# Optimization experiments

Measured on AMD Instinct MI355X. Metric: run time of the kernel, lower is better.

Reference implementation:

```python
import jax, jax.numpy as jnp
import numpy as np

B, T, I, H = 64, 1024, 256, 512


def setup_inputs() -> dict:
    key = jax.random.key(0)
    ks = jax.random.split(key, 5)
    s = 1.0 / np.sqrt(H)  # PyTorch LSTM init scale (uniform(-s, s)); we use scaled normal
    return {
        "x": jax.random.normal(ks[0], (B, T, I), dtype=jnp.float32),
        "w_ih": jax.random.normal(ks[1], (4 * H, I), dtype=jnp.float32) * s,
        "w_hh": jax.random.normal(ks[2], (4 * H, H), dtype=jnp.float32) * s,
        "b_ih": jax.random.normal(ks[3], (4 * H,), dtype=jnp.float32) * s,
        "b_hh": jax.random.normal(ks[4], (4 * H,), dtype=jnp.float32) * s,
    }


def _lstm(x, w_ih, w_hh, b_ih, b_hh):
    # x: [B, T, I]. Precompute input projections for all timesteps at once.
    pre = jnp.einsum("bti,gi->btg", x, w_ih) + b_ih + b_hh  # [B, T, 4H]
    pre = jnp.swapaxes(pre, 0, 1)  # [T, B, 4H] for scan over time

    h0 = jnp.zeros((x.shape[0], H), dtype=x.dtype)
    c0 = jnp.zeros((x.shape[0], H), dtype=x.dtype)

    def step(carry, pre_t):
        h, c = carry
        gates = pre_t + h @ w_hh.T  # [B, 4H]
        i, f, g, o = jnp.split(gates, 4, axis=-1)  # PyTorch gate order: i, f, g, o
        i = jax.nn.sigmoid(i)
        f = jax.nn.sigmoid(f)
        g = jnp.tanh(g)
        o = jax.nn.sigmoid(o)
        c = f * c + i * g
        h = o * jnp.tanh(c)
        return (h, c), h

    (h_n, c_n), hs = jax.lax.scan(step, (h0, c0), pre)
    out = jnp.swapaxes(hs, 0, 1)  # [B, T, H] (batch_first=True)
    return out, (h_n[None], c_n[None])  # h_n/c_n: [num_layers=1, B, H]


def reference(x, w_ih, w_hh, b_ih, b_hh):
    return _lstm(x, w_ih, w_hh, b_ih, b_hh)
```

## Files before the change

kernel.cpp:

```cpp
#include <hip/hip_runtime.h>
#include <cstdint>
#include <cstddef>


#define NBATCH 64
#define TSTEPS 1024
#define IDIM   256
#define HDIM   512
#define KDIM   768
#define WS     776
#define ABUF_USHORT (16 * WS)
#define SMEM_BYTES  (2 * ABUF_USHORT * 2)

#define HB_WORDS 32768

typedef __attribute__((ext_vector_type(8))) short short8x;
typedef __attribute__((ext_vector_type(4))) float f32x4;

__device__ __forceinline__ float sigmoid_f(float v) {
    return 1.0f / (1.0f + __expf(-v));
}
__device__ __forceinline__ float tanh_f(float v) {
    float a = fabsf(v);
    float e = __expf(-2.0f * a);
    float r = (1.0f - e) / (1.0f + e);
    return v >= 0.0f ? r : -r;
}
__device__ __forceinline__ unsigned short f2bf(float f) {
    unsigned int u = __float_as_uint(f);
    return (unsigned short)((u + 0x7fffu + ((u >> 16) & 1u)) >> 16);
}
__device__ __forceinline__ unsigned long long pack4(float4 v) {
    unsigned long long b0 = f2bf(v.x), b1 = f2bf(v.y), b2 = f2bf(v.z), b3 = f2bf(v.w);
    return b0 | (b1 << 16) | (b2 << 32) | (b3 << 48);
}

__global__ void __launch_bounds__(256, 1) lstm_persistent(
    const float* __restrict__ x,
    const float* __restrict__ w_ih,
    const float* __restrict__ w_hh,
    const float* __restrict__ b_ih,
    const float* __restrict__ b_hh,
    float* __restrict__ out,
    unsigned int* __restrict__ h_tb)
{
    const int tid = threadIdx.x;
    const int wg  = blockIdx.x;
    const int bg  = wg >> 4;
    const int hg  = wg & 15;

    extern __shared__ char smem[];
    unsigned short* a0 = (unsigned short*)smem;
    unsigned short* a1 = a0 + ABUF_USHORT;

    const int wv   = tid >> 6;
    const int lane = tid & 63;
    const int ln   = lane & 15;
    const int q    = lane >> 4;

    short8x af0[24], af1[24];
    float bias0[4], bias1[4];
    #pragma unroll
    for (int tau = 0; tau < 2; ++tau) {
        const int T  = wv * 2 + tau;
        const int gr = (ln & 3) * HDIM + hg * 32 + T * 4 + (ln >> 2);
        #pragma unroll
        for (int s = 0; s < 24; ++s) {
            const float* src = (s < 8)
                ? (w_ih + (size_t)gr * IDIM + (s * 32 + q * 8))
                : (w_hh + (size_t)gr * HDIM + ((s - 8) * 32 + q * 8));
            float4 v0 = *(const float4*)(src);
            float4 v1 = *(const float4*)(src + 4);
            union { short8x v; unsigned long long u[2]; } tmp;
            tmp.u[0] = pack4(v0);
            tmp.u[1] = pack4(v1);
            if (tau == 0) af0[s] = tmp.v; else af1[s] = tmp.v;
        }
        const int hid = hg * 32 + T * 4 + q;
        #pragma unroll
        for (int j = 0; j < 4; ++j) {
            float bv = b_ih[j * HDIM + hid] + b_hh[j * HDIM + hid];
            if (tau == 0) bias0[j] = bv; else bias1[j] = bv;
        }
    }

    const int sn  = tid >> 4;
    const int sj  = tid & 15;
    const int gbn = bg * 16 + sn;
    const float* xbase = x + (size_t)gbn * TSTEPS * IDIM + sj * 16;

    const size_t hb_lane = (size_t)(bg * 16 + ln) * HDIM + hg * 32 + wv * 8 + q;
    float c0 = 0.0f, c1 = 0.0f, h0f = 0.0f, h1f = 0.0f;

    const unsigned long long tagmask = 0xffff0000ffff0000ull;

    for (int t = 0; t < TSTEPS; ++t) {
        unsigned short* abuf = (t & 1) ? a1 : a0;
        unsigned short* axp  = abuf + sn * WS + sj * 16;
        unsigned short* ahp  = abuf + sn * WS + IDIM + sj * 32;

        {
            const float* xp = xbase + (size_t)t * IDIM;
            float4 v0 = *(const float4*)(xp);
            float4 v1 = *(const float4*)(xp + 4);
            float4 v2 = *(const float4*)(xp + 8);
            float4 v3 = *(const float4*)(xp + 12);
            *(unsigned long long*)(axp + 0)  = pack4(v0);
            *(unsigned long long*)(axp + 4)  = pack4(v1);
            *(unsigned long long*)(axp + 8)  = pack4(v2);
            *(unsigned long long*)(axp + 12) = pack4(v3);
        }

        if (t > 0) {
            const unsigned long long* hp = (const unsigned long long*)
                (h_tb + (size_t)(t & 1) * HB_WORDS + (size_t)gbn * HDIM + sj * 32);
            unsigned long long hv[16];
            const unsigned long long tagpat =
                ((unsigned long long)(unsigned)t << 48) |
                ((unsigned long long)(unsigned)t << 16);
            unsigned pend = 0xffffu;
            while (pend) {
                unsigned np = 0;
                #pragma unroll
                for (int u = 0; u < 16; ++u) {
                    if (pend & (1u << u)) {
                        hv[u] = __hip_atomic_load(hp + u, __ATOMIC_RELAXED,
                                                  __HIP_MEMORY_SCOPE_AGENT);
                    }
                }
                #pragma unroll
                for (int u = 0; u < 16; ++u) {
                    if ((pend & (1u << u)) && (hv[u] & tagmask) != tagpat)
                        np |= (1u << u);
                }
                pend = np;
            }
            unsigned int pk[16];
            #pragma unroll
            for (int u = 0; u < 16; ++u) {
                pk[u] = (unsigned int)(hv[u] & 0xffffu)
                      | ((unsigned int)((hv[u] >> 32) & 0xffffu) << 16);
            }
            unsigned int* ahp32 = (unsigned int*)ahp;
            #pragma unroll
            for (int v = 0; v < 4; ++v) {
                uint4 w4 = make_uint4(pk[4*v], pk[4*v+1], pk[4*v+2], pk[4*v+3]);
                *(uint4*)(ahp32 + 4*v) = w4;
            }
            if (sn == ((hg + t) & 15)) {
                float* op = out + ((size_t)gbn * TSTEPS + (t - 1)) * HDIM + sj * 32;
                #pragma unroll
                for (int v = 0; v < 8; ++v) {
                    unsigned int w0 = pk[2*v], w1 = pk[2*v+1];
                    f32x4 f4;
                    f4[0] = __uint_as_float(w0 << 16);
                    f4[1] = __uint_as_float(w0 & 0xffff0000u);
                    f4[2] = __uint_as_float(w1 << 16);
                    f4[3] = __uint_as_float(w1 & 0xffff0000u);
                    __builtin_nontemporal_store(f4, (f32x4*)(op + 4*v));
                }
            }
        } else {
            unsigned int* ahp32 = (unsigned int*)ahp;
            uint4 z = make_uint4(0u, 0u, 0u, 0u);
            #pragma unroll
            for (int v = 0; v < 4; ++v) *(uint4*)(ahp32 + 4*v) = z;
        }
        __syncthreads();

        const unsigned short* Bbase = abuf + (size_t)ln * WS + q * 8;
        f32x4 acc0 = {0.f, 0.f, 0.f, 0.f};
        f32x4 acc1 = {0.f, 0.f, 0.f, 0.f};
        #pragma unroll
        for (int s = 0; s < 24; ++s) {
            short8x bf = *(const short8x*)(Bbase + s * 32);
            acc0 = __builtin_amdgcn_mfma_f32_16x16x32_bf16(af0[s], bf, acc0, 0, 0, 0);
            acc1 = __builtin_amdgcn_mfma_f32_16x16x32_bf16(af1[s], bf, acc1, 0, 0, 0);
        }

        const unsigned int tagw = (unsigned int)(t + 1) << 16;
        unsigned int* hb = h_tb + (size_t)((t + 1) & 1) * HB_WORDS + hb_lane;
        {
            float ig = sigmoid_f(acc0[0] + bias0[0]);
            float fg = sigmoid_f(acc0[1] + bias0[1]);
            float gt = tanh_f   (acc0[2] + bias0[2]);
            float og = sigmoid_f(acc0[3] + bias0[3]);
            c0  = fg * c0 + ig * gt;
            h0f = og * tanh_f(c0);
            __hip_atomic_store(hb, tagw | (unsigned int)f2bf(h0f),
                               __ATOMIC_RELAXED, __HIP_MEMORY_SCOPE_AGENT);
        }
        {
            float ig = sigmoid_f(acc1[0] + bias1[0]);
            float fg = sigmoid_f(acc1[1] + bias1[1]);
            float gt = tanh_f   (acc1[2] + bias1[2]);
            float og = sigmoid_f(acc1[3] + bias1[3]);
            c1  = fg * c1 + ig * gt;
            h1f = og * tanh_f(c1);
            __hip_atomic_store(hb + 4, tagw | (unsigned int)f2bf(h1f),
                               __ATOMIC_RELAXED, __HIP_MEMORY_SCOPE_AGENT);
        }
    }

    {
        const size_t HN_OFF = (size_t)NBATCH * TSTEPS * HDIM;
        const size_t CN_OFF = HN_OFF + (size_t)NBATCH * HDIM;
        const int gb   = bg * 16 + ln;
        const int hid0 = hg * 32 + wv * 8 + q;
        out[((size_t)gb * TSTEPS + (TSTEPS - 1)) * HDIM + hid0]     = h0f;
        out[((size_t)gb * TSTEPS + (TSTEPS - 1)) * HDIM + hid0 + 4] = h1f;
        out[HN_OFF + (size_t)gb * HDIM + hid0]     = h0f;
        out[HN_OFF + (size_t)gb * HDIM + hid0 + 4] = h1f;
        out[CN_OFF + (size_t)gb * HDIM + hid0]     = c0;
        out[CN_OFF + (size_t)gb * HDIM + hid0 + 4] = c1;
    }
}

extern "C" void kernel_launch(void* const* d_in, const int* in_sizes, int n_in,
                              void* d_out, int out_size, void* d_ws, size_t ws_size,
                              hipStream_t stream) {
    const float* x    = (const float*)d_in[0];
    const float* w_ih = (const float*)d_in[1];
    const float* w_hh = (const float*)d_in[2];
    const float* b_ih = (const float*)d_in[3];
    const float* b_hh = (const float*)d_in[4];
    float* out = (float*)d_out;

    unsigned int* h_tb = (unsigned int*)d_ws;

    (void)hipFuncSetAttribute((const void*)lstm_persistent,
                        hipFuncAttributeMaxDynamicSharedMemorySize, SMEM_BYTES);

    void* args[] = {(void*)&x, (void*)&w_ih, (void*)&w_hh, (void*)&b_ih,
                    (void*)&b_hh, (void*)&out, (void*)&h_tb};
    hipError_t err = hipLaunchCooperativeKernel((void*)lstm_persistent,
                                                dim3(64), dim3(256), args,
                                                SMEM_BYTES, stream);
    if (err != hipSuccess) {
        hipLaunchKernelGGL(lstm_persistent, dim3(64), dim3(256), SMEM_BYTES,
                           stream, x, w_ih, w_hh, b_ih, b_hh, out, h_tb);
    }
}
```

Baseline: 5.477 ms.

## Halve workgroups to 32, four hidden tiles per wave, vectorized tagged h exchange

Repartitions the persistent LSTM from 64 to 32 workgroups, so each wave holds four weight fragment sets in registers and computes 64 hidden units per workgroup. The h-exchange is rewritten with dwordx4 sc0/sc1 loads and stores of tagged words, and the bias moves to shared memory. The aim is fewer participants in the per-step cross-workgroup sync and fewer, wider memory transactions. The cost is doubled per-step MFMA work per workgroup, higher register pressure (96 fragment vectors), and fewer CUs in use.

```diff
diff --git a/kernel.cpp b/kernel.cpp
--- a/kernel.cpp
+++ b/kernel.cpp
@@ -10,12 +10,14 @@
 #define KDIM   768
 #define WS     776
 #define ABUF_USHORT (16 * WS)
-#define SMEM_BYTES  (2 * ABUF_USHORT * 2)
+#define BIAS_OFF    (2 * ABUF_USHORT * 2)
+#define SMEM_BYTES  (BIAS_OFF + 1024)
 
 #define HB_WORDS 32768
 
 typedef __attribute__((ext_vector_type(8))) short short8x;
 typedef __attribute__((ext_vector_type(4))) float f32x4;
+typedef __attribute__((ext_vector_type(4))) unsigned int u32x4;
 
 __device__ __forceinline__ float sigmoid_f(float v) {
     return 1.0f / (1.0f + __expf(-v));
@@ -33,6 +35,9 @@
 __device__ __forceinline__ unsigned long long pack4(float4 v) {
     unsigned long long b0 = f2bf(v.x), b1 = f2bf(v.y), b2 = f2bf(v.z), b3 = f2bf(v.w);
     return b0 | (b1 << 16) | (b2 << 32) | (b3 << 48);
+}
+__device__ __forceinline__ unsigned int pklo(unsigned int a, unsigned int b) {
+    return (a & 0xffffu) | (b << 16);
 }
 
 __global__ void __launch_bounds__(256, 1) lstm_persistent(
@@ -46,42 +51,49 @@
 {
     const int tid = threadIdx.x;
     const int wg  = blockIdx.x;
-    const int bg  = wg >> 4;
-    const int hg  = wg & 15;
+    const int bg  = wg >> 3;
+    const int hg  = wg & 7;
 
     extern __shared__ char smem[];
     unsigned short* a0 = (unsigned short*)smem;
     unsigned short* a1 = a0 + ABUF_USHORT;
+    float* bias_s = (float*)(smem + BIAS_OFF);
 
     const int wv   = tid >> 6;
     const int lane = tid & 63;
     const int ln   = lane & 15;
     const int q    = lane >> 4;
 
-    short8x af0[24], af1[24];
-    float bias0[4], bias1[4];
-    #pragma unroll
-    for (int tau = 0; tau < 2; ++tau) {
-        const int T  = wv * 2 + tau;
-        const int gr = (ln & 3) * HDIM + hg * 32 + T * 4 + (ln >> 2);
+    short8x af0[24], af1[24], af2[24], af3[24];
+    {
+        const int grb = (ln & 3) * HDIM + hg * 64 + wv * 16 + (ln >> 2) * 4;
+#define LOADW(AF, TAU)                                                        \
+        {                                                                     \
+            const int gr = grb + (TAU);                                       \
+            _Pragma("unroll")                                                 \
+            for (int s = 0; s < 24; ++s) {                                    \
+                const float* src = (s < 8)                                    \
+                    ? (w_ih + (size_t)gr * IDIM + (s * 32 + q * 8))           \
+                    : (w_hh + (size_t)gr * HDIM + ((s - 8) * 32 + q * 8));    \
+                float4 v0 = *(const float4*)(src);                            \
+                float4 v1 = *(const float4*)(src + 4);                        \
+                union { short8x v; unsigned long long u[2]; } tmp;            \
+                tmp.u[0] = pack4(v0);                                         \
+                tmp.u[1] = pack4(v1);                                         \
+                AF[s] = tmp.v;                                                \
+            }                                                                 \
+        }
+        LOADW(af0, 0) LOADW(af1, 1) LOADW(af2, 2) LOADW(af3, 3)
+#undef LOADW
+    }
+
+    if (ln < 4) {
+        const int tau = ln;
+        const int hid = hg * 64 + wv * 16 + q * 4 + tau;
         #pragma unroll
-        for (int s = 0; s < 24; ++s) {
-            const float* src = (s < 8)
-                ? (w_ih + (size_t)gr * IDIM + (s * 32 + q * 8))
-                : (w_hh + (size_t)gr * HDIM + ((s - 8) * 32 + q * 8));
-            float4 v0 = *(const float4*)(src);
-            float4 v1 = *(const float4*)(src + 4);
-            union { short8x v; unsigned long long u[2]; } tmp;
-            tmp.u[0] = pack4(v0);
-            tmp.u[1] = pack4(v1);
-            if (tau == 0) af0[s] = tmp.v; else af1[s] = tmp.v;
-        }
-        const int hid = hg * 32 + T * 4 + q;
-        #pragma unroll
-        for (int j = 0; j < 4; ++j) {
-            float bv = b_ih[j * HDIM + hid] + b_hh[j * HDIM + hid];
-            if (tau == 0) bias0[j] = bv; else bias1[j] = bv;
-        }
+        for (int j = 0; j < 4; ++j)
+            bias_s[(wv * 4 + q) * 16 + tau * 4 + j] =
+                b_ih[j * HDIM + hid] + b_hh[j * HDIM + hid];
     }
 
     const int sn  = tid >> 4;
@@ -89,15 +101,14 @@
     const int gbn = bg * 16 + sn;
     const float* xbase = x + (size_t)gbn * TSTEPS * IDIM + sj * 16;
 
-    const size_t hb_lane = (size_t)(bg * 16 + ln) * HDIM + hg * 32 + wv * 8 + q;
-    float c0 = 0.0f, c1 = 0.0f, h0f = 0.0f, h1f = 0.0f;
-
-    const unsigned long long tagmask = 0xffff0000ffff0000ull;
+    const size_t hb_off = (size_t)(bg * 16 + ln) * HDIM + hg * 64 + wv * 16 + q * 4;
+    float c0 = 0.f, c1 = 0.f, c2 = 0.f, c3 = 0.f;
+    float hf0 = 0.f, hf1 = 0.f, hf2 = 0.f, hf3 = 0.f;
 
     for (int t = 0; t < TSTEPS; ++t) {
         unsigned short* abuf = (t & 1) ? a1 : a0;
         unsigned short* axp  = abuf + sn * WS + sj * 16;
-        unsigned short* ahp  = abuf + sn * WS + IDIM + sj * 32;
+        unsigned int*   ahp32 = (unsigned int*)(abuf + sn * WS + IDIM + sj * 32);
 
         {
             const float* xp = xbase + (size_t)t * IDIM;
@@ -112,93 +123,100 @@
         }
 
         if (t > 0) {
-            const unsigned long long* hp = (const unsigned long long*)
-                (h_tb + (size_t)(t & 1) * HB_WORDS + (size_t)gbn * HDIM + sj * 32);
-            unsigned long long hv[16];
-            const unsigned long long tagpat =
-                ((unsigned long long)(unsigned)t << 48) |
-                ((unsigned long long)(unsigned)t << 16);
-            unsigned pend = 0xffffu;
+            const unsigned int* hp =
+                h_tb + (size_t)(t & 1) * HB_WORDS + (size_t)gbn * HDIM + sj * 32;
+            u32x4 hv[8];
+            const unsigned int tagw = (unsigned int)t << 16;
+            unsigned pend = 0xffu;
             while (pend) {
+                #pragma unroll
+                for (int u = 0; u < 8; ++u) {
+                    if (pend & (1u << u)) {
+                        asm volatile("global_load_dwordx4 %0, %1, off sc0 sc1"
+                                     : "=v"(hv[u]) : "v"(hp + u * 4) : "memory");
+                    }
+                }
+                asm volatile("s_waitcnt vmcnt(0)" ::: "memory");
+                __builtin_amdgcn_sched_barrier(0);
                 unsigned np = 0;
                 #pragma unroll
-                for (int u = 0; u < 16; ++u) {
+                for (int u = 0; u < 8; ++u) {
                     if (pend & (1u << u)) {
-                        hv[u] = __hip_atomic_load(hp + u, __ATOMIC_RELAXED,
-                                                  __HIP_MEMORY_SCOPE_AGENT);
+                        unsigned m = ((hv[u][0] ^ tagw) | (hv[u][1] ^ tagw) |
+                                      (hv[u][2] ^ tagw) | (hv[u][3] ^ tagw))
+                                     & 0xffff0000u;
+                        if (m) np |= (1u << u);
                     }
-                }
-                #pragma unroll
-                for (int u = 0; u < 16; ++u) {
-                    if ((pend & (1u << u)) && (hv[u] & tagmask) != tagpat)
-                        np |= (1u << u);
                 }
                 pend = np;
             }
-            unsigned int pk[16];
-            #pragma unroll
-            for (int u = 0; u < 16; ++u) {
-                pk[u] = (unsigned int)(hv[u] & 0xffffu)
-                      | ((unsigned int)((hv[u] >> 32) & 0xffffu) << 16);
-            }
-            unsigned int* ahp32 = (unsigned int*)ahp;
             #pragma unroll
             for (int v = 0; v < 4; ++v) {
-                uint4 w4 = make_uint4(pk[4*v], pk[4*v+1], pk[4*v+2], pk[4*v+3]);
-                *(uint4*)(ahp32 + 4*v) = w4;
+                u32x4 a = hv[2 * v], b = hv[2 * v + 1];
+                u32x4 w4;
+                w4[0] = pklo(a[0], a[1]);
+                w4[1] = pklo(a[2], a[3]);
+                w4[2] = pklo(b[0], b[1]);
+                w4[3] = pklo(b[2], b[3]);
+                *(u32x4*)(ahp32 + 4 * v) = w4;
             }
-            if (sn == ((hg + t) & 15)) {
+            if ((sn & 7) == ((hg + t) & 7)) {
                 float* op = out + ((size_t)gbn * TSTEPS + (t - 1)) * HDIM + sj * 32;
                 #pragma unroll
-                for (int v = 0; v < 8; ++v) {
-                    unsigned int w0 = pk[2*v], w1 = pk[2*v+1];
+                for (int u = 0; u < 8; ++u) {
+                    u32x4 h4 = hv[u];
                     f32x4 f4;
-                    f4[0] = __uint_as_float(w0 << 16);
-                    f4[1] = __uint_as_float(w0 & 0xffff0000u);
-                    f4[2] = __uint_as_float(w1 << 16);
-                    f4[3] = __uint_as_float(w1 & 0xffff0000u);
-                    __builtin_nontemporal_store(f4, (f32x4*)(op + 4*v));
+                    f4[0] = __uint_as_float(h4[0] << 16);
+                    f4[1] = __uint_as_float(h4[1] << 16);
+                    f4[2] = __uint_as_float(h4[2] << 16);
+                    f4[3] = __uint_as_float(h4[3] << 16);
+                    __builtin_nontemporal_store(f4, (f32x4*)(op + 4 * u));
                 }
             }
         } else {
-            unsigned int* ahp32 = (unsigned int*)ahp;
-            uint4 z = make_uint4(0u, 0u, 0u, 0u);
+            u32x4 z = {0u, 0u, 0u, 0u};
             #pragma unroll
-            for (int v = 0; v < 4; ++v) *(uint4*)(ahp32 + 4*v) = z;
+            for (int v = 0; v < 4; ++v) *(u32x4*)(ahp32 + 4 * v) = z;
         }
         __syncthreads();
 
         const unsigned short* Bbase = abuf + (size_t)ln * WS + q * 8;
-        f32x4 acc0 = {0.f, 0.f, 0.f, 0.f};
-        f32x4 acc1 = {0.f, 0.f, 0.f, 0.f};
+        f32x4 ac0 = {0.f, 0.f, 0.f, 0.f};
+        f32x4 ac1 = {0.f, 0.f, 0.f, 0.f};
+        f32x4 ac2 = {0.f, 0.f, 0.f, 0.f};
+        f32x4 ac3 = {0.f, 0.f, 0.f, 0.f};
         #pragma unroll
         for (int s = 0; s < 24; ++s) {
             short8x bf = *(const short8x*)(Bbase + s * 32);
-            acc0 = __builtin_amdgcn_mfma_f32_16x16x32_bf16(af0[s], bf, acc0, 0, 0, 0);
-            acc1 = __builtin_amdgcn_mfma_f32_16x16x32_bf16(af1[s], bf, acc1, 0, 0, 0);
-        }
-
-        const unsigned int tagw = (unsigned int)(t + 1) << 16;
-        unsigned int* hb = h_tb + (size_t)((t + 1) & 1) * HB_WORDS + hb_lane;
+            ac0 = __builtin_amdgcn_mfma_f32_16x16x32_bf16(af0[s], bf, ac0, 0, 0, 0);
+            ac1 = __builtin_amdgcn_mfma_f32_16x16x32_bf16(af1[s], bf, ac1, 0, 0, 0);
+            ac2 = __builtin_amdgcn_mfma_f32_16x16x32_bf16(af2[s], bf, ac2, 0, 0, 0);
+            ac3 = __builtin_amdgcn_mfma_f32_16x16x32_bf16(af3[s], bf, ac3, 0, 0, 0);
+        }
+
+        const unsigned int tagw1 = (unsigned int)(t + 1) << 16;
+        const float* bsl = bias_s + (wv * 4 + q) * 16;
+        u32x4 pub;
+#define ACT(ACC, TAU, CREF, HREF)                                             \
+        {                                                                     \
+            f32x4 bs = *(const f32x4*)(bsl + (TAU) * 4);                      \
+            float ig = sigmoid_f(ACC[0] + bs[0]);                             \
+            float fg = sigmoid_f(ACC[1] + bs[1]);                             \
+            float gt = tanh_f   (ACC[2] + bs[2]);                             \
+            float og = sigmoid_f(ACC[3] + bs[3]);                             \
+            CREF = fg * CREF + ig * gt;                                       \
+            HREF = og * tanh_f(CREF);                                         \
+            pub[TAU] = tagw1 | (unsigned int)f2bf(HREF);                      \
+        }
+        ACT(ac0, 0, c0, hf0)
+        ACT(ac1, 1, c1, hf1)
+        ACT(ac2, 2, c2, hf2)
+        ACT(ac3, 3, c3, hf3)
+#undef ACT
         {
-            float ig = sigmoid_f(acc0[0] + bias0[0]);
-            float fg = sigmoid_f(acc0[1] + bias0[1]);
-            float gt = tanh_f   (acc0[2] + bias0[2]);
-            float og = sigmoid_f(acc0[3] + bias0[3]);
-            c0  = fg * c0 + ig * gt;
-            h0f = og * tanh_f(c0);
-            __hip_atomic_store(hb, tagw | (unsigned int)f2bf(h0f),
-                               __ATOMIC_RELAXED, __HIP_MEMORY_SCOPE_AGENT);
-        }
-        {
-            float ig = sigmoid_f(acc1[0] + bias1[0]);
-            float fg = sigmoid_f(acc1[1] + bias1[1]);
-            float gt = tanh_f   (acc1[2] + bias1[2]);
-            float og = sigmoid_f(acc1[3] + bias1[3]);
-            c1  = fg * c1 + ig * gt;
-            h1f = og * tanh_f(c1);
-            __hip_atomic_store(hb + 4, tagw | (unsigned int)f2bf(h1f),
-                               __ATOMIC_RELAXED, __HIP_MEMORY_SCOPE_AGENT);
+            unsigned int* hb = h_tb + (size_t)((t + 1) & 1) * HB_WORDS + hb_off;
+            asm volatile("global_store_dwordx4 %0, %1, off sc0 sc1"
+                         :: "v"(hb), "v"(pub) : "memory");
         }
     }
 
@@ -206,13 +224,12 @@
         const size_t HN_OFF = (size_t)NBATCH * TSTEPS * HDIM;
         const size_t CN_OFF = HN_OFF + (size_t)NBATCH * HDIM;
         const int gb   = bg * 16 + ln;
-        const int hid0 = hg * 32 + wv * 8 + q;
-        out[((size_t)gb * TSTEPS + (TSTEPS - 1)) * HDIM + hid0]     = h0f;
-        out[((size_t)gb * TSTEPS + (TSTEPS - 1)) * HDIM + hid0 + 4] = h1f;
-        out[HN_OFF + (size_t)gb * HDIM + hid0]     = h0f;
-        out[HN_OFF + (size_t)gb * HDIM + hid0 + 4] = h1f;
-        out[CN_OFF + (size_t)gb * HDIM + hid0]     = c0;
-        out[CN_OFF + (size_t)gb * HDIM + hid0 + 4] = c1;
+        const int hid0 = hg * 64 + wv * 16 + q * 4;
+        f32x4 hv4 = {hf0, hf1, hf2, hf3};
+        f32x4 cv4 = {c0, c1, c2, c3};
+        *(f32x4*)(out + ((size_t)gb * TSTEPS + (TSTEPS - 1)) * HDIM + hid0) = hv4;
+        *(f32x4*)(out + HN_OFF + (size_t)gb * HDIM + hid0) = hv4;
+        *(f32x4*)(out + CN_OFF + (size_t)gb * HDIM + hid0) = cv4;
     }
 }
 
@@ -234,10 +251,10 @@
     void* args[] = {(void*)&x, (void*)&w_ih, (void*)&w_hh, (void*)&b_ih,
                     (void*)&b_hh, (void*)&out, (void*)&h_tb};
     hipError_t err = hipLaunchCooperativeKernel((void*)lstm_persistent,
-                                                dim3(64), dim3(256), args,
+                                                dim3(32), dim3(256), args,
                                                 SMEM_BYTES, stream);
     if (err != hipSuccess) {
-        hipLaunchKernelGGL(lstm_persistent, dim3(64), dim3(256), SMEM_BYTES,
+        hipLaunchKernelGGL(lstm_persistent, dim3(32), dim3(256), SMEM_BYTES,
                            stream, x, w_ih, w_hh, b_ih, b_hh, out, h_tb);
     }
 }
```

After: 5.357 ms. -2.2%, faster.
